# Kernel optimization log

Hardware: AMD Instinct MI355X
Metric: run time of the kernel (lower is better)

## Reference

```python
import jax, jax.numpy as jnp
import numpy as np

N, E = 50000, 800000
CUR, HID, OUT = 128, 96, 128
NEG_SLOPE = 0.01  # F.leaky_relu default


def setup_inputs() -> dict:
    key = jax.random.key(0)
    ks = jax.random.split(key, 12)
    inv = lambda d: 1.0 / np.sqrt(d)
    return {
        "h": jax.random.normal(ks[0], (N, CUR), jnp.float32),
        "x": jax.random.normal(ks[1], (N, CUR), jnp.float32),
        "edge_index": jax.random.randint(ks[2], (2, E), 0, N, dtype=jnp.int64),
        "edge_weight": jax.random.uniform(ks[3], (E,), jnp.float32),
        # preprocessor_x: Linear(cur_dim, hidden_dim)
        "pre_W": jax.random.uniform(ks[4], (CUR, HID), jnp.float32, -inv(CUR), inv(CUR)),
        "pre_b": jax.random.uniform(ks[5], (HID,), jnp.float32, -inv(CUR), inv(CUR)),
        # SAGEConv(hidden, out): lin_l (neighbor, with bias) + lin_r (root, no bias)
        "sage_Wl": jax.random.uniform(ks[6], (HID, OUT), jnp.float32, -inv(HID), inv(HID)),
        "sage_bl": jnp.zeros((OUT,), jnp.float32),
        "sage_Wr": jax.random.uniform(ks[7], (HID, OUT), jnp.float32, -inv(HID), inv(HID)),
        # ARMAConv(hidden, out) with K=1 stacks, T=1 layers (PyG defaults)
        "arma_W": jax.random.uniform(ks[8], (HID, OUT), jnp.float32, -inv(HID), inv(HID)),
        "arma_V": jax.random.uniform(ks[9], (HID, OUT), jnp.float32, -inv(HID), inv(HID)),
        "arma_b": jnp.zeros((OUT,), jnp.float32),
    }


def _cell(x, src, dst, edge_weight, pre_W, pre_b,
          sage_Wl, sage_bl, sage_Wr, arma_W, arma_V, arma_b):
    n = x.shape[0]
    xh = x @ pre_W + pre_b  # [N, HID]

    # ---- SAGEConv: mean aggregation of edge-weighted neighbor features ----
    msg = xh[src] * edge_weight[:, None]                     # [E, HID]
    aggr = jax.ops.segment_sum(msg, dst, num_segments=n)     # [N, HID]
    cnt = jax.ops.segment_sum(jnp.ones_like(edge_weight), dst, num_segments=n)
    mean = aggr / jnp.maximum(cnt, 1.0)[:, None]
    o_sage = mean @ sage_Wl + sage_bl + xh @ sage_Wr         # [N, OUT]

    # ---- ARMAConv (K=1, T=1): ReLU(L_hat (x W) + x V + b) ----
    deg = jax.ops.segment_sum(edge_weight, dst, num_segments=n)
    dinv = jnp.where(deg > 0, jax.lax.rsqrt(jnp.maximum(deg, 1e-30)), 0.0)
    norm = dinv[src] * edge_weight * dinv[dst]               # [E]
    xw = xh @ arma_W                                         # [N, OUT]
    prop = jax.ops.segment_sum(xw[src] * norm[:, None], dst, num_segments=n)
    o_arma = jax.nn.relu(prop + xh @ arma_V + arma_b)        # [N, OUT]

    o1 = jax.nn.leaky_relu(o_sage, NEG_SLOPE)
    o2 = jax.nn.leaky_relu(o_arma, NEG_SLOPE)
    return jax.nn.relu(o1 + o2)


def reference(h, x, edge_index, edge_weight, pre_W, pre_b,
              sage_Wl, sage_bl, sage_Wr, arma_W, arma_V, arma_b):
    src, dst = edge_index[0], edge_index[1]
    his = x
    o3 = _cell(x, src, dst, edge_weight, pre_W, pre_b,
               sage_Wl, sage_bl, sage_Wr, arma_W, arma_V, arma_b)
    return (his, o3)
```

## Files before the change

kernel.cpp:

```cpp
#include <hip/hip_runtime.h>


typedef __attribute__((ext_vector_type(8))) short bf16x8;
typedef __attribute__((ext_vector_type(4))) float f32x4;

__device__ __forceinline__ float bf2f(unsigned short u) {
    return __uint_as_float(((unsigned)u) << 16);
}
__device__ __forceinline__ unsigned short f2bf(float f) {
    unsigned u = __float_as_uint(f);
    return (unsigned short)((u + 0x7FFFu + ((u >> 16) & 1u)) >> 16);
}

__global__ void k_flag(const unsigned* __restrict__ ei, int* __restrict__ flag) {
    __shared__ int bad;
    if (threadIdx.x == 0) bad = 0;
    __syncthreads();
    unsigned w = ei[2 * threadIdx.x + 1];
    if (w != 0) atomicAdd(&bad, 1);
    __syncthreads();
    if (threadIdx.x == 0) *flag = (bad == 0) ? 1 : 0;
}

__device__ __forceinline__ int edge_src(const int* ei, int e, int E, int flag) {
    return flag ? ei[2 * e] : ei[e];
}
__device__ __forceinline__ int edge_dst(const int* ei, int e, int E, int flag) {
    return flag ? ei[2 * (E + e)] : ei[E + e];
}

__global__ void k_wprep(const float* __restrict__ Wl, const float* __restrict__ Wr,
                        const float* __restrict__ Wa, const float* __restrict__ Va,
                        const float* __restrict__ preW,
                        unsigned short* __restrict__ Wf_s,
                        unsigned short* __restrict__ Wf_a,
                        unsigned short* __restrict__ Wfp,
                        int4* __restrict__ cnt4, int nz4) {
    int tid = blockIdx.x * blockDim.x + threadIdx.x;
    if (tid < 6144) {
        int mat = tid / 3072, rem = tid % 3072;
        int kstep = rem / 512, rem2 = rem % 512;
        int g = rem2 / 128, j = rem2 % 128;
        int k0 = kstep * 32 + g * 8;
        const float* Wtop = mat ? Wa : Wl;
        const float* Wbot = mat ? Va : Wr;
        unsigned short* dst = (mat ? Wf_a : Wf_s) + (((size_t)(kstep * 4 + g) * 128 + j) * 8);
#pragma unroll
        for (int kk = 0; kk < 8; kk++) {
            int k = k0 + kk;
            float v = (k < 96) ? Wtop[k * 128 + j] : Wbot[(k - 96) * 128 + j];
            dst[kk] = f2bf(v);
        }
    } else if (tid < 7680) {
        int rem = tid - 6144;
        int kstep = rem / 384, rem2 = rem % 384;
        int g = rem2 / 96, j = rem2 % 96;
        int k0 = kstep * 32 + g * 8;
        unsigned short* dst = Wfp + (((size_t)(kstep * 4 + g) * 96 + j) * 8);
#pragma unroll
        for (int kk = 0; kk < 8; kk++) dst[kk] = f2bf(preW[(k0 + kk) * 96 + j]);
    } else if (tid >= 8192 && tid < 8192 + nz4) {
        cnt4[tid - 8192] = make_int4(0, 0, 0, 0);
    }
}

__global__ __launch_bounds__(256) void k_xh(const float* __restrict__ x,
                                            const unsigned short* __restrict__ Wfp,
                                            const float* __restrict__ b,
                                            unsigned short* __restrict__ xhbf,
                                            float* __restrict__ out0, int N) {
    __shared__ unsigned short X[64][136];
    int t = threadIdx.x;
    int nb = blockIdx.x * 64;
    for (int u = t; u < 2048; u += 256) {
        int row = u >> 5, q = u & 31;
        long gn = nb + row;
        float4 v = make_float4(0.f, 0.f, 0.f, 0.f);
        if (gn < N) {
            v = ((const float4*)(x + gn * 128))[q];
            ((float4*)(out0 + gn * 128))[q] = v;
        }
        unsigned short* p = &X[row][q * 4];
        p[0] = f2bf(v.x); p[1] = f2bf(v.y); p[2] = f2bf(v.z); p[3] = f2bf(v.w);
    }
    __syncthreads();
    int lane = t & 63, w = t >> 6;
    int lr = lane & 15, lg = lane >> 4;
    bf16x8 a[4];
#pragma unroll
    for (int ks = 0; ks < 4; ks++)
        a[ks] = *(const bf16x8*)&X[w * 16 + lr][ks * 32 + lg * 8];
    for (int jt = 0; jt < 6; jt++) {
        f32x4 acc = {0.f, 0.f, 0.f, 0.f};
#pragma unroll
        for (int ks = 0; ks < 4; ks++) {
            bf16x8 bf = *(const bf16x8*)(Wfp + (((size_t)(ks * 4 + lg) * 96 + jt * 16 + lr) * 8));
            acc = __builtin_amdgcn_mfma_f32_16x16x32_bf16(a[ks], bf, acc, 0, 0, 0);
        }
        int h = jt * 16 + lr;
        float bb = b[h];
#pragma unroll
        for (int r = 0; r < 4; r++) {
            long n = nb + w * 16 + lg * 4 + r;
            if (n < N) xhbf[n * 96 + h] = f2bf(acc[r] + bb);
        }
    }
}

__global__ void k_count(const int* __restrict__ ei, int* __restrict__ cnt_i,
                        int* __restrict__ pos, int E, const int* __restrict__ flagp) {
    int e = blockIdx.x * blockDim.x + threadIdx.x;
    if (e >= E) return;
    int flag = *flagp;
    int d = edge_dst(ei, e, E, flag);
    pos[e] = atomicAdd(&cnt_i[d], 1);
}

__global__ void k_scan_blk(const int* __restrict__ cnt, int* __restrict__ offs,
                           int* __restrict__ bsum, int N) {
    __shared__ int sh[256];
    int t = threadIdx.x;
    int n = blockIdx.x * 256 + t;
    int v = (n < N) ? cnt[n] : 0;
    sh[t] = v;
    __syncthreads();
    for (int off = 1; off < 256; off <<= 1) {
        int add = (t >= off) ? sh[t - off] : 0;
        __syncthreads();
        sh[t] += add;
        __syncthreads();
    }
    if (n < N) offs[n + 1] = sh[t];
    if (t == 255) bsum[blockIdx.x] = sh[255];
    if (blockIdx.x == 0 && t == 0) offs[0] = 0;
}

__global__ void k_scan_top(int* __restrict__ bsum, int nb) {
    __shared__ int sh[256];
    int t = threadIdx.x;
    sh[t] = (t < nb) ? bsum[t] : 0;
    __syncthreads();
    for (int off = 1; off < 256; off <<= 1) {
        int add = (t >= off) ? sh[t - off] : 0;
        __syncthreads();
        sh[t] += add;
        __syncthreads();
    }
    bsum[t] = sh[t];
}

__global__ void k_scan_add(int* __restrict__ offs, const int* __restrict__ bsum, int N) {
    int t = threadIdx.x;
    int n = blockIdx.x * 256 + t;
    if (n < N && blockIdx.x > 0) offs[n + 1] += bsum[blockIdx.x - 1];
}

__global__ void k_fill(const int* __restrict__ ei, const float* __restrict__ ew,
                       const int* __restrict__ offs, const int* __restrict__ pos,
                       int* __restrict__ esrc, float* __restrict__ eww, int E,
                       const int* __restrict__ flagp) {
    int e = blockIdx.x * blockDim.x + threadIdx.x;
    if (e >= E) return;
    int flag = *flagp;
    int s = edge_src(ei, e, E, flag);
    int d = edge_dst(ei, e, E, flag);
    int idx = offs[d] + pos[e];
    esrc[idx] = s;
    eww[idx] = ew[e];
}

__global__ void k_degcsr(const float* __restrict__ eww, const int* __restrict__ offs,
                         float* __restrict__ dinv, float* __restrict__ minv, int N) {
    int n = blockIdx.x * blockDim.x + threadIdx.x;
    if (n >= N) return;
    int beg = offs[n], end = offs[n + 1];
    float dg = 0.f;
    for (int e = beg; e < end; e++) dg += eww[e];
    dinv[n] = dg > 0.f ? rsqrtf(fmaxf(dg, 1e-30f)) : 0.f;
    minv[n] = 1.f / fmaxf((float)(end - beg), 1.f);
}

__global__ __launch_bounds__(256) void k_gather(
    const int* __restrict__ esrc, const float* __restrict__ eww,
    const unsigned short* __restrict__ xhbf, const int* __restrict__ offs,
    const float* __restrict__ dinv, const float* __restrict__ minv,
    unsigned short* __restrict__ meanbf, unsigned short* __restrict__ propbf, int N) {
    int lane = threadIdx.x & 63;
    int d = __builtin_amdgcn_readfirstlane(blockIdx.x * 4 + (threadIdx.x >> 6));
    if (d >= N) return;
    int beg = offs[d], end = offs[d + 1];
    bool act = lane < 48;
    int col = 2 * lane;
    float s0 = 0.f, s1 = 0.f, a0 = 0.f, a1 = 0.f;
    int e = beg;
    for (; e + 8 <= end; e += 8) {
        int idx[8]; float wgt[8], dv[8]; unsigned v[8];
#pragma unroll
        for (int q = 0; q < 8; q++) { idx[q] = esrc[e + q]; wgt[q] = eww[e + q]; }
#pragma unroll
        for (int q = 0; q < 8; q++) dv[q] = dinv[idx[q]];
#pragma unroll
        for (int q = 0; q < 8; q++)
            v[q] = act ? *(const unsigned*)(xhbf + (size_t)idx[q] * 96 + col) : 0u;
#pragma unroll
        for (int q = 0; q < 8; q++) {
            float x0 = bf2f((unsigned short)(v[q] & 0xffff));
            float x1 = bf2f((unsigned short)(v[q] >> 16));
            float w2 = wgt[q], dw = dv[q] * w2;
            s0 += w2 * x0; s1 += w2 * x1;
            a0 += dw * x0; a1 += dw * x1;
        }
    }
    for (; e + 4 <= end; e += 4) {
        int idx[4]; float wgt[4], dv[4]; unsigned v[4];
#pragma unroll
        for (int q = 0; q < 4; q++) { idx[q] = esrc[e + q]; wgt[q] = eww[e + q]; }
#pragma unroll
        for (int q = 0; q < 4; q++) dv[q] = dinv[idx[q]];
#pragma unroll
        for (int q = 0; q < 4; q++)
            v[q] = act ? *(const unsigned*)(xhbf + (size_t)idx[q] * 96 + col) : 0u;
#pragma unroll
        for (int q = 0; q < 4; q++) {
            float x0 = bf2f((unsigned short)(v[q] & 0xffff));
            float x1 = bf2f((unsigned short)(v[q] >> 16));
            float w2 = wgt[q], dw = dv[q] * w2;
            s0 += w2 * x0; s1 += w2 * x1;
            a0 += dw * x0; a1 += dw * x1;
        }
    }
    for (; e < end; e++) {
        int s = esrc[e];
        float w2 = eww[e];
        float ds = dinv[s];
        if (act) {
            unsigned v = *(const unsigned*)(xhbf + (size_t)s * 96 + col);
            float x0 = bf2f((unsigned short)(v & 0xffff));
            float x1 = bf2f((unsigned short)(v >> 16));
            s0 += w2 * x0; s1 += w2 * x1;
            a0 += ds * w2 * x0; a1 += ds * w2 * x1;
        }
    }
    if (act) {
        float mi = minv[d], di = dinv[d];
        unsigned mo = (unsigned)f2bf(s0 * mi) | ((unsigned)f2bf(s1 * mi) << 16);
        unsigned po = (unsigned)f2bf(a0 * di) | ((unsigned)f2bf(a1 * di) << 16);
        *(unsigned*)(meanbf + (size_t)d * 96 + col) = mo;
        *(unsigned*)(propbf + (size_t)d * 96 + col) = po;
    }
}

__global__ __launch_bounds__(256) void k_out(
    const unsigned short* __restrict__ meanbf, const unsigned short* __restrict__ propbf,
    const unsigned short* __restrict__ xhbf, const unsigned short* __restrict__ Wf_s,
    const unsigned short* __restrict__ Wf_a, const float* __restrict__ bl,
    const float* __restrict__ ba, float* __restrict__ out, int N) {
    __shared__ unsigned short A[3][64][104];
    int t = threadIdx.x;
    int nb = blockIdx.x * 64;
    for (int u = t; u < 2304; u += 256) {
        int arr = u / 768, rem = u - arr * 768;
        int row = rem / 12, c = rem - row * 12;
        long gn = nb + row;
        const unsigned short* src = (arr == 0) ? meanbf : (arr == 1) ? propbf : xhbf;
        float4 v = (gn < N) ? *(const float4*)(src + gn * 96 + c * 8)
                            : make_float4(0.f, 0.f, 0.f, 0.f);
        *(float4*)&A[arr][row][c * 8] = v;
    }
    __syncthreads();
    int lane = t & 63, w = t >> 6;
    int lr = lane & 15, lg = lane >> 4;
    bf16x8 am[3], ap[3], ax[3];
#pragma unroll
    for (int ks = 0; ks < 3; ks++) {
        int row = w * 16 + lr, kc = ks * 32 + lg * 8;
        am[ks] = *(const bf16x8*)&A[0][row][kc];
        ap[ks] = *(const bf16x8*)&A[1][row][kc];
        ax[ks] = *(const bf16x8*)&A[2][row][kc];
    }
    for (int jt = 0; jt < 8; jt++) {
        f32x4 accS = {0.f, 0.f, 0.f, 0.f};
        f32x4 accA = {0.f, 0.f, 0.f, 0.f};
#pragma unroll
        for (int ks = 0; ks < 3; ks++) {
            size_t boffS = ((size_t)(ks * 4 + lg) * 128 + jt * 16 + lr) * 8;
            size_t boffS2 = ((size_t)((ks + 3) * 4 + lg) * 128 + jt * 16 + lr) * 8;
            bf16x8 b0 = *(const bf16x8*)(Wf_s + boffS);
            bf16x8 b1 = *(const bf16x8*)(Wf_s + boffS2);
            bf16x8 b2 = *(const bf16x8*)(Wf_a + boffS);
            bf16x8 b3 = *(const bf16x8*)(Wf_a + boffS2);
            accS = __builtin_amdgcn_mfma_f32_16x16x32_bf16(am[ks], b0, accS, 0, 0, 0);
            accS = __builtin_amdgcn_mfma_f32_16x16x32_bf16(ax[ks], b1, accS, 0, 0, 0);
            accA = __builtin_amdgcn_mfma_f32_16x16x32_bf16(ap[ks], b2, accA, 0, 0, 0);
            accA = __builtin_amdgcn_mfma_f32_16x16x32_bf16(ax[ks], b3, accA, 0, 0, 0);
        }
        int j = jt * 16 + lr;
        float blj = bl[j], baj = ba[j];
#pragma unroll
        for (int r = 0; r < 4; r++) {
            long n = nb + w * 16 + lg * 4 + r;
            if (n < N) {
                float os = accS[r] + blj;
                float oa = fmaxf(accA[r] + baj, 0.f);
                float o1 = os > 0.f ? os : 0.01f * os;
                float o2 = oa > 0.f ? oa : 0.01f * oa;
                out[n * 128 + j] = fmaxf(o1 + o2, 0.f);
            }
        }
    }
}

extern "C" void kernel_launch(void* const* d_in, const int* in_sizes, int n_in,
                              void* d_out, int out_size, void* d_ws, size_t ws_size,
                              hipStream_t stream) {
    const float* x    = (const float*)d_in[1];
    const int*   ei   = (const int*)d_in[2];
    const float* ew   = (const float*)d_in[3];
    const float* preW = (const float*)d_in[4];
    const float* preb = (const float*)d_in[5];
    const float* Wl   = (const float*)d_in[6];
    const float* bl   = (const float*)d_in[7];
    const float* Wr   = (const float*)d_in[8];
    const float* Wa   = (const float*)d_in[9];
    const float* Va   = (const float*)d_in[10];
    const float* ba   = (const float*)d_in[11];

    const int N = in_sizes[1] / 128;
    const int E = in_sizes[3];
    const int NB = (N + 255) / 256;

    char* w = (char*)d_ws;
    unsigned short* xhbf   = (unsigned short*)w; w += (size_t)N * 96 * 2;
    unsigned short* meanbf = (unsigned short*)w; w += (size_t)N * 96 * 2;
    unsigned short* propbf = (unsigned short*)w; w += (size_t)N * 96 * 2;
    unsigned short* Wf_s   = (unsigned short*)w; w += (size_t)6 * 4 * 128 * 8 * 2;
    unsigned short* Wf_a   = (unsigned short*)w; w += (size_t)6 * 4 * 128 * 8 * 2;
    unsigned short* Wfp    = (unsigned short*)w; w += (size_t)4 * 4 * 96 * 8 * 2;
    int*   esrc = (int*)w;   w += (size_t)E * 4;
    float* eww  = (float*)w; w += (size_t)E * 4;
    int*   pos  = (int*)w;   w += (size_t)E * 4;
    int*   cnt_i = (int*)w;  w += (size_t)N * 4;
    float* dinv = (float*)w; w += (size_t)N * 4;
    float* minv = (float*)w; w += (size_t)N * 4;
    int*   offs = (int*)w;   w += (size_t)(N + 1) * 4;
    int*   bsum = (int*)w;   w += 256 * 4;
    int*   flag = (int*)w;

    const int nz4 = (N + 3) / 4;
    const int wprep_blocks = (8192 + nz4 + 255) / 256;

    k_flag<<<1, 1024, 0, stream>>>((const unsigned*)ei, flag);
    k_wprep<<<wprep_blocks, 256, 0, stream>>>(Wl, Wr, Wa, Va, preW, Wf_s, Wf_a, Wfp,
                                              (int4*)cnt_i, nz4);
    k_xh<<<(N + 63) / 64, 256, 0, stream>>>(x, Wfp, preb, xhbf, (float*)d_out, N);
    k_count<<<(E + 255) / 256, 256, 0, stream>>>(ei, cnt_i, pos, E, flag);
    k_scan_blk<<<NB, 256, 0, stream>>>(cnt_i, offs, bsum, N);
    k_scan_top<<<1, 256, 0, stream>>>(bsum, NB);
    k_scan_add<<<NB, 256, 0, stream>>>(offs, bsum, N);
    k_fill<<<(E + 255) / 256, 256, 0, stream>>>(ei, ew, offs, pos, esrc, eww, E, flag);
    k_degcsr<<<NB, 256, 0, stream>>>(eww, offs, dinv, minv, N);
    k_gather<<<(N + 3) / 4, 256, 0, stream>>>(esrc, eww, xhbf, offs, dinv,
                                              minv, meanbf, propbf, N);
    k_out<<<(N + 63) / 64, 256, 0, stream>>>(meanbf, propbf, xhbf, Wf_s, Wf_a,
                                             bl, ba, (float*)d_out + (size_t)N * 128, N);
}
```

Before: 161.2 us.

## Fuse flag check into wprep, merge xh and edge count, shard degree counters

Folds the int64-detection flag kernel into the weight-prep launch, and merges the edge-counting pass into the xh GEMM kernel as extra blocks so the two independent jobs share one launch. Per-destination counters are split into 8 shards chosen by block index, which spreads out atomic contention, and the scan computes per-shard offsets that the fill kernel uses. The cost is 8x more counter memory to zero and read in the scan, plus an extra sdelta array and an extra indexed read per edge in fill.

Result: faster. 147.5 us (-8.5%).

```diff
diff --git a/kernel.cpp b/kernel.cpp
--- a/kernel.cpp
+++ b/kernel.cpp
@@ -12,16 +12,6 @@
     return (unsigned short)((u + 0x7FFFu + ((u >> 16) & 1u)) >> 16);
 }
 
-__global__ void k_flag(const unsigned* __restrict__ ei, int* __restrict__ flag) {
-    __shared__ int bad;
-    if (threadIdx.x == 0) bad = 0;
-    __syncthreads();
-    unsigned w = ei[2 * threadIdx.x + 1];
-    if (w != 0) atomicAdd(&bad, 1);
-    __syncthreads();
-    if (threadIdx.x == 0) *flag = (bad == 0) ? 1 : 0;
-}
-
 __device__ __forceinline__ int edge_src(const int* ei, int e, int E, int flag) {
     return flag ? ei[2 * e] : ei[e];
 }
@@ -29,14 +19,31 @@
     return flag ? ei[2 * (E + e)] : ei[E + e];
 }
 
-__global__ void k_wprep(const float* __restrict__ Wl, const float* __restrict__ Wr,
+__global__ void k_wprep(const unsigned* __restrict__ eiu,
+                        const float* __restrict__ Wl, const float* __restrict__ Wr,
                         const float* __restrict__ Wa, const float* __restrict__ Va,
                         const float* __restrict__ preW,
                         unsigned short* __restrict__ Wf_s,
                         unsigned short* __restrict__ Wf_a,
                         unsigned short* __restrict__ Wfp,
+                        int* __restrict__ flag,
                         int4* __restrict__ cnt4, int nz4) {
-    int tid = blockIdx.x * blockDim.x + threadIdx.x;
+    if (blockIdx.x == 0) {
+        __shared__ int bad;
+        if (threadIdx.x == 0) bad = 0;
+        __syncthreads();
+        int nb = 0;
+#pragma unroll
+        for (int q = 0; q < 4; q++) {
+            unsigned w = eiu[2 * (threadIdx.x * 4 + q) + 1];
+            if (w != 0) nb++;
+        }
+        if (nb) atomicAdd(&bad, nb);
+        __syncthreads();
+        if (threadIdx.x == 0) *flag = (bad == 0) ? 1 : 0;
+        return;
+    }
+    int tid = (blockIdx.x - 1) * blockDim.x + threadIdx.x;
     if (tid < 6144) {
         int mat = tid / 3072, rem = tid % 3072;
         int kstep = rem / 512, rem2 = rem % 512;
@@ -64,12 +71,24 @@
     }
 }
 
-__global__ __launch_bounds__(256) void k_xh(const float* __restrict__ x,
-                                            const unsigned short* __restrict__ Wfp,
-                                            const float* __restrict__ b,
-                                            unsigned short* __restrict__ xhbf,
-                                            float* __restrict__ out0, int N) {
+__global__ __launch_bounds__(256) void k_xh_count(
+    const float* __restrict__ x, const unsigned short* __restrict__ Wfp,
+    const float* __restrict__ b, unsigned short* __restrict__ xhbf,
+    float* __restrict__ out0, int N, int xhBlocks,
+    const int* __restrict__ ei, int* __restrict__ cntS, int* __restrict__ pos,
+    int E, const int* __restrict__ flagp) {
     __shared__ unsigned short X[64][136];
+    if (blockIdx.x >= xhBlocks) {
+        int e = (blockIdx.x - xhBlocks) * 256 + threadIdx.x;
+        if (e < E) {
+            int flag = *flagp;
+            int d = edge_dst(ei, e, E, flag);
+            int shard = blockIdx.x & 7;
+            int lp = atomicAdd(&cntS[(size_t)shard * N + d], 1);
+            pos[e] = (lp << 3) | shard;
+        }
+        return;
+    }
     int t = threadIdx.x;
     int nb = blockIdx.x * 64;
     for (int u = t; u < 2048; u += 256) {
@@ -107,22 +126,22 @@
     }
 }
 
-__global__ void k_count(const int* __restrict__ ei, int* __restrict__ cnt_i,
-                        int* __restrict__ pos, int E, const int* __restrict__ flagp) {
-    int e = blockIdx.x * blockDim.x + threadIdx.x;
-    if (e >= E) return;
-    int flag = *flagp;
-    int d = edge_dst(ei, e, E, flag);
-    pos[e] = atomicAdd(&cnt_i[d], 1);
-}
-
-__global__ void k_scan_blk(const int* __restrict__ cnt, int* __restrict__ offs,
-                           int* __restrict__ bsum, int N) {
+__global__ void k_scan_blk(const int* __restrict__ cntS, int* __restrict__ sdelta,
+                           int* __restrict__ offs, int* __restrict__ bsum, int N) {
     __shared__ int sh[256];
     int t = threadIdx.x;
     int n = blockIdx.x * 256 + t;
-    int v = (n < N) ? cnt[n] : 0;
-    sh[t] = v;
+    int total = 0;
+    if (n < N) {
+        int run = 0;
+#pragma unroll
+        for (int s = 0; s < 8; s++) {
+            sdelta[(size_t)s * N + n] = run;
+            run += cntS[(size_t)s * N + n];
+        }
+        total = run;
+    }
+    sh[t] = total;
     __syncthreads();
     for (int off = 1; off < 256; off <<= 1) {
         int add = (t >= off) ? sh[t - off] : 0;
@@ -156,15 +175,18 @@
 }
 
 __global__ void k_fill(const int* __restrict__ ei, const float* __restrict__ ew,
-                       const int* __restrict__ offs, const int* __restrict__ pos,
-                       int* __restrict__ esrc, float* __restrict__ eww, int E,
+                       const int* __restrict__ offs, const int* __restrict__ sdelta,
+                       const int* __restrict__ pos, int* __restrict__ esrc,
+                       float* __restrict__ eww, int E, int N,
                        const int* __restrict__ flagp) {
     int e = blockIdx.x * blockDim.x + threadIdx.x;
     if (e >= E) return;
     int flag = *flagp;
     int s = edge_src(ei, e, E, flag);
     int d = edge_dst(ei, e, E, flag);
-    int idx = offs[d] + pos[e];
+    int pp = pos[e];
+    int shard = pp & 7, lp = pp >> 3;
+    int idx = offs[d] + sdelta[(size_t)shard * N + d] + lp;
     esrc[idx] = s;
     eww[idx] = ew[e];
 }
@@ -336,28 +358,32 @@
     unsigned short* Wf_s   = (unsigned short*)w; w += (size_t)6 * 4 * 128 * 8 * 2;
     unsigned short* Wf_a   = (unsigned short*)w; w += (size_t)6 * 4 * 128 * 8 * 2;
     unsigned short* Wfp    = (unsigned short*)w; w += (size_t)4 * 4 * 96 * 8 * 2;
-    int*   esrc = (int*)w;   w += (size_t)E * 4;
-    float* eww  = (float*)w; w += (size_t)E * 4;
-    int*   pos  = (int*)w;   w += (size_t)E * 4;
-    int*   cnt_i = (int*)w;  w += (size_t)N * 4;
-    float* dinv = (float*)w; w += (size_t)N * 4;
-    float* minv = (float*)w; w += (size_t)N * 4;
-    int*   offs = (int*)w;   w += (size_t)(N + 1) * 4;
-    int*   bsum = (int*)w;   w += 256 * 4;
-    int*   flag = (int*)w;
-
-    const int nz4 = (N + 3) / 4;
-    const int wprep_blocks = (8192 + nz4 + 255) / 256;
-
-    k_flag<<<1, 1024, 0, stream>>>((const unsigned*)ei, flag);
-    k_wprep<<<wprep_blocks, 256, 0, stream>>>(Wl, Wr, Wa, Va, preW, Wf_s, Wf_a, Wfp,
-                                              (int4*)cnt_i, nz4);
-    k_xh<<<(N + 63) / 64, 256, 0, stream>>>(x, Wfp, preb, xhbf, (float*)d_out, N);
-    k_count<<<(E + 255) / 256, 256, 0, stream>>>(ei, cnt_i, pos, E, flag);
-    k_scan_blk<<<NB, 256, 0, stream>>>(cnt_i, offs, bsum, N);
+    int*   esrc   = (int*)w;   w += (size_t)E * 4;
+    float* eww    = (float*)w; w += (size_t)E * 4;
+    int*   pos    = (int*)w;   w += (size_t)E * 4;
+    int*   cntS   = (int*)w;   w += (size_t)8 * N * 4;
+    int*   sdelta = (int*)w;   w += (size_t)8 * N * 4;
+    float* dinv   = (float*)w; w += (size_t)N * 4;
+    float* minv   = (float*)w; w += (size_t)N * 4;
+    int*   offs   = (int*)w;   w += (size_t)(N + 1) * 4;
+    int*   bsum   = (int*)w;   w += 256 * 4;
+    int*   flag   = (int*)w;
+
+    const int nz4 = (8 * N + 3) / 4;
+    const int wprep_blocks = 1 + (8192 + nz4 + 255) / 256;
+    const int xhBlocks = (N + 63) / 64;
+    const int cntBlocks = (E + 255) / 256;
+
+    k_wprep<<<wprep_blocks, 256, 0, stream>>>((const unsigned*)ei, Wl, Wr, Wa, Va,
+                                              preW, Wf_s, Wf_a, Wfp, flag,
+                                              (int4*)cntS, nz4);
+    k_xh_count<<<xhBlocks + cntBlocks, 256, 0, stream>>>(
+        x, Wfp, preb, xhbf, (float*)d_out, N, xhBlocks, ei, cntS, pos, E, flag);
+    k_scan_blk<<<NB, 256, 0, stream>>>(cntS, sdelta, offs, bsum, N);
     k_scan_top<<<1, 256, 0, stream>>>(bsum, NB);
     k_scan_add<<<NB, 256, 0, stream>>>(offs, bsum, N);
-    k_fill<<<(E + 255) / 256, 256, 0, stream>>>(ei, ew, offs, pos, esrc, eww, E, flag);
+    k_fill<<<(E + 255) / 256, 256, 0, stream>>>(ei, ew, offs, sdelta, pos, esrc,
+                                                eww, E, N, flag);
     k_degcsr<<<NB, 256, 0, stream>>>(eww, offs, dinv, minv, N);
     k_gather<<<(N + 3) / 4, 256, 0, stream>>>(esrc, eww, xhbf, offs, dinv,
                                               minv, meanbf, propbf, N);
```
